# Optimization experiments

Hardware: AMD Instinct MI355X
Metric: run time of the kernel (lower is better)

## Reference

```python
import jax, jax.numpy as jnp
import numpy as np


def _dilate(x, ker):
    """Grayscale (max-plus) dilation, TF tf.nn.dilation2d semantics, SAME pad, stride 1.

    x:   [B,H,W,C] or [B,H,W,C,F]
    ker: [kh,kw,C,F]
    out: [B,H,W,C,F] = max_{dy,dx} x_pad[b, h+dy, w+dx, c(,f)] + ker[dy,dx,c,f]
    """
    kh, kw = ker.shape[0], ker.shape[1]
    pt, pl = (kh - 1) // 2, (kw - 1) // 2
    pb, pr = kh - 1 - pt, kw - 1 - pl
    if x.ndim == 4:
        x = x[..., None]  # broadcast over filter axis
    B, H, W = x.shape[0], x.shape[1], x.shape[2]
    xp = jnp.pad(x, ((0, 0), (pt, pb), (pl, pr), (0, 0), (0, 0)),
                 constant_values=-jnp.inf)
    out = None
    for dy in range(kh):
        for dx in range(kw):
            v = xp[:, dy:dy + H, dx:dx + W] + ker[dy, dx]  # [B,H,W,C,F]
            out = v if out is None else jnp.maximum(out, v)
    return out


def _erode(x, ker):
    # TF identity: erosion2d(v, f) = -dilation2d(-v, spatially-flipped f)
    return -_dilate(-x, ker[::-1, ::-1])


def _opening_p4(x, kernel):
    # x: [B,4,H,W,C], kernel: [kh,kw,3,C,F]
    kero = jnp.stack([jnp.rot90(kernel[:, :, 2], 3, axes=(0, 1)),
                      kernel[:, :, 1],
                      jnp.rot90(kernel[:, :, 0], 1, axes=(0, 1))], axis=2)
    y = jnp.concatenate([x[:, -1:], x, x[:, :1]], axis=1)  # wrap group axis -> [B,6,H,W,C]
    ero = []
    for j in range(4):
        kr = jnp.rot90(kero, j, axes=(0, 1))  # [kh,kw,3,C,F]
        d = jnp.stack([_erode(y[:, j + k], kr[:, :, k]) for k in range(3)], axis=-1)
        ero.append(jnp.min(d, axis=-1))  # min over SE depth -> [B,H,W,C,F]
    ero = jnp.stack(ero, axis=1)  # [B,4,H,W,C,F]
    ep = jnp.concatenate([ero[:, -1:], ero, ero[:, :1]], axis=1)  # [B,6,H,W,C,F]
    outs = []
    for j in range(4):
        kr = jnp.rot90(kernel, j, axes=(0, 1))
        d = jnp.stack([_dilate(ep[:, j + k], kr[:, :, k]) for k in range(3)], axis=-1)
        outs.append(jnp.max(d, axis=-1))  # max over SE depth -> [B,H,W,C,F]
    open_res = jnp.stack(outs, axis=1)  # [B,4,H,W,C,F]
    return jnp.sum(open_res, axis=-2)   # sum over input channels -> [B,4,H,W,F]


def setup_inputs() -> dict:
    key = jax.random.key(0)
    k1, k2 = jax.random.split(key)
    x = jax.random.normal(k1, (4, 4, 64, 64, 8), dtype=jnp.float32)
    kernel = jax.random.normal(k2, (3, 3, 3, 8, 16), dtype=jnp.float32) * 0.1
    return {"x": x, "kernel": kernel}


def reference(x, kernel):
    return _opening_p4(x, kernel)
```

## Files before the change

kernel.cpp:

```cpp
#include <hip/hip_runtime.h>


#define HH 64
#define WW 64
#define NEG_INF (-__builtin_inff())
#define POS_INF (__builtin_inff())

#define ROT_G(G, A, B, I, J) do { switch (G) { \
    case 0:  I = (A);     J = (B);     break; \
    case 1:  I = (B);     J = 2 - (A); break; \
    case 2:  I = 2 - (A); J = 2 - (B); break; \
    default: I = 2 - (B); J = (A);     break; } } while (0)

typedef _Float16 hv4 __attribute__((ext_vector_type(4)));

__device__ __forceinline__ hv4 f4_to_hv4(float4 v) {
    hv4 r;
    r.x = (_Float16)v.x; r.y = (_Float16)v.y;
    r.z = (_Float16)v.z; r.w = (_Float16)v.w;
    return r;
}

__global__ __launch_bounds__(256) void erode_t(const float* __restrict__ x,
                                               const float* __restrict__ ker,
                                               hv4* __restrict__ ero) {
    __shared__ __align__(16) float xs[9 * 8 * 68];

    const int tid = threadIdx.x;
    const int h = blockIdx.x & 63;
    const int g = (blockIdx.x >> 6) & 3;
    const int b = blockIdx.x >> 8;

    const float4* x4 = (const float4*)x;
    const float4* ker4 = (const float4*)ker;

    for (int t = tid; t < 1188; t += 256) {
        int q01 = t & 1;
        int u = t >> 1;
        int wp = u % 66;
        int v = u / 66;
        int r = v % 3;
        int p = v / 3;
        int g2 = (g + p + 3) & 3;
        int h2 = h - 1 + r;
        int w2 = wp - 1;
        float4 vv;
        if ((unsigned)h2 < HH && (unsigned)w2 < WW)
            vv = x4[(((b * 4 + g2) * HH + h2) * WW + w2) * 2 + q01];
        else
            vv = make_float4(POS_INF, POS_INF, POS_INF, POS_INF);
        int rowb = (p * 3 + r) * 8 + q01 * 4;
        xs[(rowb + 0) * 68 + wp] = vv.x;
        xs[(rowb + 1) * 68 + wp] = vv.y;
        xs[(rowb + 2) * 68 + wp] = vv.z;
        xs[(rowb + 3) * 68 + wp] = vv.w;
    }
    __syncthreads();

    const int q = tid & 3;
    const int c = (tid >> 2) & 7;
    const int slot = tid >> 5;
    const float4* xs4 = (const float4*)xs;

    float4 acc[8];
#pragma unroll
    for (int i = 0; i < 8; ++i)
        acc[i] = make_float4(POS_INF, POS_INF, POS_INF, POS_INF);

#pragma unroll
    for (int k2 = 0; k2 < 3; ++k2) {
        float4 ke9[9];
#pragma unroll
        for (int t9 = 0; t9 < 9; ++t9) {
            int dy = t9 / 3, dx = t9 % 3;
            int a0 = 2 - dy, b0 = 2 - dx;
            int i, jj;
            ROT_G(g, a0, b0, i, jj);
            int ka, kb, kc;
            if (k2 == 0)      { ka = 2 - jj; kb = i;      kc = 2; }
            else if (k2 == 1) { ka = i;      kb = jj;     kc = 1; }
            else              { ka = jj;     kb = 2 - i;  kc = 0; }
            ke9[t9] = ker4[((ka * 3 + kb) * 3 + kc) * 32 + c * 4 + q];
        }
#pragma unroll
        for (int dy = 0; dy < 3; ++dy) {
            const int base4 = ((k2 * 3 + dy) * 8 + c) * 17 + slot * 2;
            float4 xa = xs4[base4];
            float4 xb = xs4[base4 + 1];
            float4 xc = xs4[base4 + 2];
            float xw[12] = {xa.x, xa.y, xa.z, xa.w,
                            xb.x, xb.y, xb.z, xb.w,
                            xc.x, xc.y, xc.z, xc.w};
#pragma unroll
            for (int dx = 0; dx < 3; ++dx) {
                float4 kv = ke9[dy * 3 + dx];
#pragma unroll
                for (int i = 0; i < 8; ++i) {
                    float v = xw[i + dx];
                    acc[i].x = fminf(acc[i].x, v - kv.x);
                    acc[i].y = fminf(acc[i].y, v - kv.y);
                    acc[i].z = fminf(acc[i].z, v - kv.z);
                    acc[i].w = fminf(acc[i].w, v - kv.w);
                }
            }
        }
    }

    const int row = (b * 4 + g) * HH + h;
    const size_t obase = ((size_t)row * 66 + slot * 8 + 1) * 32 + c * 4 + q;
#pragma unroll
    for (int i = 0; i < 8; ++i)
        ero[obase + (size_t)i * 32] = f4_to_hv4(acc[i]);

    const hv4 ninf = {(_Float16)NEG_INF, (_Float16)NEG_INF,
                      (_Float16)NEG_INF, (_Float16)NEG_INF};
    if (tid < 32)
        ero[(size_t)row * 66 * 32 + tid] = ninf;
    else if (tid < 64)
        ero[((size_t)row * 66 + 65) * 32 + (tid - 32)] = ninf;
}

__global__ __launch_bounds__(256) void dilate_t2(const hv4* __restrict__ ero,
                                                 const float* __restrict__ ker,
                                                 float* __restrict__ out) {
    __shared__ __align__(16) hv4 es[4 * 6 * 10 * 32];

    const int tid = threadIdx.x;
    const int ws = blockIdx.x & 7;
    const int hs = (blockIdx.x >> 3) & 15;
    const int b = blockIdx.x >> 7;

    {
        const float4* ero4 = (const float4*)ero;
        float4* es4 = (float4*)es;
        const float nf = __uint_as_float(0xFC00FC00u);
        const float4 ninf4 = make_float4(nf, nf, nf, nf);
        for (int t = tid; t < 3840; t += 256) {
            const int cq2 = t & 15;
            const int rest = t >> 4;
            const int wp10 = rest % 10;
            const int ge = rest / 10;
            const int ei = ge % 6;
            const int gsrc = ge / 6;
            const int er = hs * 4 - 1 + ei;
            float4 v = ninf4;
            if ((unsigned)er < HH)
                v = ero4[(((b * 4 + gsrc) * HH + er) * 66 + ws * 8 + wp10) * 16 + cq2];
            es4[rest * 16 + cq2] = v;
        }
    }
    __syncthreads();

    const int q = tid & 3;
    const int c = (tid >> 2) & 7;
    const int cq = tid & 31;
    const int slot = tid >> 5;
    const float4* ker4 = (const float4*)ker;

    const hv4 ninf = {(_Float16)NEG_INF, (_Float16)NEG_INF,
                      (_Float16)NEG_INF, (_Float16)NEG_INF};
    hv4 acc[4][4];
#pragma unroll
    for (int j = 0; j < 4; ++j)
#pragma unroll
        for (int r = 0; r < 4; ++r)
            acc[j][r] = ninf;

#pragma unroll
    for (int j = 0; j < 4; ++j) {
#pragma unroll
        for (int k = 0; k < 3; ++k) {
            const int gsrc = (j + k + 3) & 3;
            hv4 kd9[9];
#pragma unroll
            for (int t9 = 0; t9 < 9; ++t9) {
                int dy = t9 / 3, dx = t9 % 3;
                int i, jj;
                ROT_G(j, dy, dx, i, jj);
                kd9[t9] = f4_to_hv4(ker4[((i * 3 + jj) * 3 + k) * 32 + cq]);
            }
            const int pbase = gsrc * 1920 + slot * 32 + cq;
#pragma unroll
            for (int ei = 0; ei < 6; ++ei) {
                const int rb = pbase + ei * 320;
                hv4 e0 = es[rb];
                hv4 e1 = es[rb + 32];
                hv4 e2 = es[rb + 64];
#pragma unroll
                for (int dy = 0; dy < 3; ++dy) {
                    const int rr = ei - dy;
                    if (rr < 0 || rr >= 4) continue;
                    acc[j][rr] = __builtin_elementwise_max(acc[j][rr], e0 + kd9[dy * 3 + 0]);
                    acc[j][rr] = __builtin_elementwise_max(acc[j][rr], e1 + kd9[dy * 3 + 1]);
                    acc[j][rr] = __builtin_elementwise_max(acc[j][rr], e2 + kd9[dy * 3 + 2]);
                }
            }
        }
    }

    float4* out4 = (float4*)out;
    const int w = ws * 8 + slot;
#pragma unroll
    for (int j = 0; j < 4; ++j) {
        const int rowb = (b * 4 + j) * HH + hs * 4;
#pragma unroll
        for (int rr = 0; rr < 4; ++rr) {
            float4 s = make_float4((float)acc[j][rr].x, (float)acc[j][rr].y,
                                   (float)acc[j][rr].z, (float)acc[j][rr].w);
#pragma unroll
            for (int off = 4; off <= 16; off <<= 1) {
                s.x += __shfl_xor(s.x, off, 64);
                s.y += __shfl_xor(s.y, off, 64);
                s.z += __shfl_xor(s.z, off, 64);
                s.w += __shfl_xor(s.w, off, 64);
            }
            if (c == 0)
                out4[((size_t)(rowb + rr) * WW + w) * 4 + q] = s;
        }
    }
}

__global__ __launch_bounds__(256, 3) void opening_fused_fb(
    const float* __restrict__ x, const float* __restrict__ ker, float* __restrict__ out)
{
    __shared__ __align__(16) float xs[8 * 4 * 144];
    __shared__ float4 es4[4 * 4 * 100];
    __shared__ float4 ke4[27 * 4 * 4];
    __shared__ float4 kd4[9 * 4 * 4];

    const int tid = threadIdx.x;
    const int tileX = blockIdx.x & 7;
    const int tileY = (blockIdx.x >> 3) & 7;
    const int j = (blockIdx.x >> 6) & 3;
    const int b = blockIdx.x >> 8;
    const float4* ker4 = (const float4*)ker;
    const float4* x4 = (const float4*)x;

    for (int t = tid; t < 1152; t += 256) {
        int q01 = t & 1;
        int cell = t >> 1;
        int g = cell / 144;
        int rem = cell - g * 144;
        int r = rem / 12;
        int s = rem - r * 12;
        int h = tileY * 8 - 2 + r;
        int w = tileX * 8 - 2 + s;
        float4 v;
        if ((unsigned)h < HH && (unsigned)w < WW)
            v = x4[(((b * 4 + g) * HH + h) * WW + w) * 2 + q01];
        else
            v = make_float4(POS_INF, POS_INF, POS_INF, POS_INF);
        int c0 = q01 * 4;
        xs[((c0 + 0) * 4 + g) * 144 + rem] = v.x;
        xs[((c0 + 1) * 4 + g) * 144 + rem] = v.y;
        xs[((c0 + 2) * 4 + g) * 144 + rem] = v.z;
        xs[((c0 + 3) * 4 + g) * 144 + rem] = v.w;
    }
    __syncthreads();

    const int q_o = tid & 3;
    const int ox = (tid >> 2) & 7;
    const int oy = tid >> 5;

    float4 acc[8];
#pragma unroll
    for (int c = 0; c < 8; ++c)
        acc[c] = make_float4(NEG_INF, NEG_INF, NEG_INF, NEG_INF);

    for (int k = 0; k < 3; ++k) {
        const int gsrc = (j + k + 3) & 3;
#pragma unroll
        for (int cg = 0; cg < 2; ++cg) {
            for (int t = tid; t < 576; t += 256) {
                if (t < 432) {
                    int q = t & 3;
                    int c4 = (t >> 2) & 3;
                    int tap = t >> 4;
                    int k2 = tap % 3;
                    int dxdy = tap / 3;
                    int dx = dxdy % 3;
                    int dy = dxdy / 3;
                    int a0 = 2 - dy, b0 = 2 - dx;
                    int i, jj;
                    ROT_G(gsrc, a0, b0, i, jj);
                    int ka, kb, kc;
                    if (k2 == 0)      { ka = 2 - jj; kb = i;      kc = 2; }
                    else if (k2 == 1) { ka = i;      kb = jj;     kc = 1; }
                    else              { ka = jj;     kb = 2 - i;  kc = 0; }
                    int c = cg * 4 + c4;
                    ke4[t] = ker4[((ka * 3 + kb) * 3 + kc) * 32 + c * 4 + q];
                } else {
                    int u = t - 432;
                    int q = u & 3;
                    int c4 = (u >> 2) & 3;
                    int dydx = u >> 4;
                    int dx = dydx % 3;
                    int dy = dydx / 3;
                    int i, jj;
                    ROT_G(j, dy, dx, i, jj);
                    int c = cg * 4 + c4;
                    kd4[u] = ker4[((i * 3 + jj) * 3 + k) * 32 + c * 4 + q];
                }
            }
            __syncthreads();

            for (int it = 0; it < 2; ++it) {
                int id = tid + (it << 8);
                int c4 = id >> 7;
                int p = id & 127;
                if (p >= 100) continue;
                int ey = (p * 205) >> 11;
                int ex = p - ey * 10;
                int h_es = tileY * 8 - 1 + ey;
                int w_es = tileX * 8 - 1 + ex;
                float4 b0, b1, b2, b3;
                if ((unsigned)h_es < HH && (unsigned)w_es < WW) {
                    b0 = b1 = b2 = b3 = make_float4(POS_INF, POS_INF, POS_INF, POS_INF);
                    int c = cg * 4 + c4;
#pragma unroll
                    for (int k2 = 0; k2 < 3; ++k2) {
                        int g2 = (gsrc + k2 + 3) & 3;
                        int base = (c * 4 + g2) * 144 + ey * 12 + ex;
#pragma unroll
                        for (int dy = 0; dy < 3; ++dy)
#pragma unroll
                            for (int dx = 0; dx < 3; ++dx) {
                                float v = xs[base + dy * 12 + dx];
                                const float4* kk = &ke4[(((dy * 3 + dx) * 3 + k2) * 4 + c4) * 4];
                                float4 kv;
                                kv = kk[0];
                                b0.x = fminf(b0.x, v - kv.x); b0.y = fminf(b0.y, v - kv.y);
                                b0.z = fminf(b0.z, v - kv.z); b0.w = fminf(b0.w, v - kv.w);
                                kv = kk[1];
                                b1.x = fminf(b1.x, v - kv.x); b1.y = fminf(b1.y, v - kv.y);
                                b1.z = fminf(b1.z, v - kv.z); b1.w = fminf(b1.w, v - kv.w);
                                kv = kk[2];
                                b2.x = fminf(b2.x, v - kv.x); b2.y = fminf(b2.y, v - kv.y);
                                b2.z = fminf(b2.z, v - kv.z); b2.w = fminf(b2.w, v - kv.w);
                                kv = kk[3];
                                b3.x = fminf(b3.x, v - kv.x); b3.y = fminf(b3.y, v - kv.y);
                                b3.z = fminf(b3.z, v - kv.z); b3.w = fminf(b3.w, v - kv.w);
                            }
                    }
                } else {
                    b0 = b1 = b2 = b3 = make_float4(NEG_INF, NEG_INF, NEG_INF, NEG_INF);
                }
                int eb = (c4 * 4) * 100 + p;
                es4[eb] = b0; es4[eb + 100] = b1; es4[eb + 200] = b2; es4[eb + 300] = b3;
            }
            __syncthreads();

#pragma unroll
            for (int c4 = 0; c4 < 4; ++c4) {
                float4 a = acc[cg * 4 + c4];
#pragma unroll
                for (int dy = 0; dy < 3; ++dy)
#pragma unroll
                    for (int dx = 0; dx < 3; ++dx) {
                        int pos = (oy + dy) * 10 + (ox + dx);
                        float4 e = es4[(c4 * 4 + q_o) * 100 + pos];
                        float4 kv = kd4[(dy * 3 + dx) * 16 + c4 * 4 + q_o];
                        a.x = fmaxf(a.x, e.x + kv.x);
                        a.y = fmaxf(a.y, e.y + kv.y);
                        a.z = fmaxf(a.z, e.z + kv.z);
                        a.w = fmaxf(a.w, e.w + kv.w);
                    }
                acc[cg * 4 + c4] = a;
            }
            __syncthreads();
        }
    }

    float4 s = acc[0];
#pragma unroll
    for (int c = 1; c < 8; ++c) {
        s.x += acc[c].x; s.y += acc[c].y; s.z += acc[c].z; s.w += acc[c].w;
    }
    const int h = tileY * 8 + oy;
    const int w = tileX * 8 + ox;
    ((float4*)out)[(((b * 4 + j) * HH + h) * WW + w) * 4 + q_o] = s;
}

extern "C" void kernel_launch(void* const* d_in, const int* in_sizes, int n_in,
                              void* d_out, int out_size, void* d_ws, size_t ws_size,
                              hipStream_t stream) {
    const float* x = (const float*)d_in[0];
    const float* ker = (const float*)d_in[1];
    float* out = (float*)d_out;

    const size_t ero_f16_bytes = (size_t)16 * HH * 66 * 32 * 8;

    if (ws_size >= ero_f16_bytes) {
        hv4* ero = (hv4*)d_ws;
        erode_t<<<1024, 256, 0, stream>>>(x, ker, ero);
        dilate_t2<<<512, 256, 0, stream>>>(ero, ker, out);
    } else {
        opening_fused_fb<<<1024, 256, 0, stream>>>(x, ker, out);
    }
}
```

Measured before the change: 92.10 us.

## Fuse erosion and dilation into one tiled kernel with shared-memory halo

Replaces the two-kernel erode/dilate pipeline, which passed the eroded tensor through a global fp16 workspace, with a single kernel. Each 512-thread block computes the eroded 10x10 halo tile for all four groups into LDS, then dilates and channel-reduces the 8x8 output tile. This removes the global round trip and one launch. In exchange, each block recomputes the halo erosion that neighbouring tiles also compute, and the grid shrinks to 256 large blocks with heavy register use.

```diff
diff --git a/kernel.cpp b/kernel.cpp
--- a/kernel.cpp
+++ b/kernel.cpp
@@ -21,364 +21,193 @@
     return r;
 }
 
-__global__ __launch_bounds__(256) void erode_t(const float* __restrict__ x,
-                                               const float* __restrict__ ker,
-                                               hv4* __restrict__ ero) {
-    __shared__ __align__(16) float xs[9 * 8 * 68];
+__global__ __launch_bounds__(512, 2) void opening_fused_v15(
+    const float* __restrict__ x, const float* __restrict__ ker,
+    float* __restrict__ out)
+{
+    __shared__ __align__(16) float xs[4 * 8 * 148];
+    __shared__ __align__(16) hv4  es[4 * 10 * 10 * 32];
 
     const int tid = threadIdx.x;
-    const int h = blockIdx.x & 63;
-    const int g = (blockIdx.x >> 6) & 3;
-    const int b = blockIdx.x >> 8;
+    const int tx = blockIdx.x & 7;
+    const int ty = (blockIdx.x >> 3) & 7;
+    const int b  = blockIdx.x >> 6;
 
     const float4* x4 = (const float4*)x;
     const float4* ker4 = (const float4*)ker;
 
-    for (int t = tid; t < 1188; t += 256) {
-        int q01 = t & 1;
-        int u = t >> 1;
-        int wp = u % 66;
-        int v = u / 66;
-        int r = v % 3;
-        int p = v / 3;
-        int g2 = (g + p + 3) & 3;
-        int h2 = h - 1 + r;
-        int w2 = wp - 1;
-        float4 vv;
-        if ((unsigned)h2 < HH && (unsigned)w2 < WW)
-            vv = x4[(((b * 4 + g2) * HH + h2) * WW + w2) * 2 + q01];
-        else
-            vv = make_float4(POS_INF, POS_INF, POS_INF, POS_INF);
-        int rowb = (p * 3 + r) * 8 + q01 * 4;
-        xs[(rowb + 0) * 68 + wp] = vv.x;
-        xs[(rowb + 1) * 68 + wp] = vv.y;
-        xs[(rowb + 2) * 68 + wp] = vv.z;
-        xs[(rowb + 3) * 68 + wp] = vv.w;
-    }
-    __syncthreads();
-
-    const int q = tid & 3;
-    const int c = (tid >> 2) & 7;
-    const int slot = tid >> 5;
-    const float4* xs4 = (const float4*)xs;
-
-    float4 acc[8];
-#pragma unroll
-    for (int i = 0; i < 8; ++i)
-        acc[i] = make_float4(POS_INF, POS_INF, POS_INF, POS_INF);
-
-#pragma unroll
-    for (int k2 = 0; k2 < 3; ++k2) {
-        float4 ke9[9];
-#pragma unroll
-        for (int t9 = 0; t9 < 9; ++t9) {
-            int dy = t9 / 3, dx = t9 % 3;
-            int a0 = 2 - dy, b0 = 2 - dx;
-            int i, jj;
-            ROT_G(g, a0, b0, i, jj);
-            int ka, kb, kc;
-            if (k2 == 0)      { ka = 2 - jj; kb = i;      kc = 2; }
-            else if (k2 == 1) { ka = i;      kb = jj;     kc = 1; }
-            else              { ka = jj;     kb = 2 - i;  kc = 0; }
-            ke9[t9] = ker4[((ka * 3 + kb) * 3 + kc) * 32 + c * 4 + q];
-        }
-#pragma unroll
-        for (int dy = 0; dy < 3; ++dy) {
-            const int base4 = ((k2 * 3 + dy) * 8 + c) * 17 + slot * 2;
-            float4 xa = xs4[base4];
-            float4 xb = xs4[base4 + 1];
-            float4 xc = xs4[base4 + 2];
-            float xw[12] = {xa.x, xa.y, xa.z, xa.w,
-                            xb.x, xb.y, xb.z, xb.w,
-                            xc.x, xc.y, xc.z, xc.w};
-#pragma unroll
-            for (int dx = 0; dx < 3; ++dx) {
-                float4 kv = ke9[dy * 3 + dx];
-#pragma unroll
-                for (int i = 0; i < 8; ++i) {
-                    float v = xw[i + dx];
-                    acc[i].x = fminf(acc[i].x, v - kv.x);
-                    acc[i].y = fminf(acc[i].y, v - kv.y);
-                    acc[i].z = fminf(acc[i].z, v - kv.z);
-                    acc[i].w = fminf(acc[i].w, v - kv.w);
-                }
-            }
-        }
-    }
-
-    const int row = (b * 4 + g) * HH + h;
-    const size_t obase = ((size_t)row * 66 + slot * 8 + 1) * 32 + c * 4 + q;
-#pragma unroll
-    for (int i = 0; i < 8; ++i)
-        ero[obase + (size_t)i * 32] = f4_to_hv4(acc[i]);
-
-    const hv4 ninf = {(_Float16)NEG_INF, (_Float16)NEG_INF,
-                      (_Float16)NEG_INF, (_Float16)NEG_INF};
-    if (tid < 32)
-        ero[(size_t)row * 66 * 32 + tid] = ninf;
-    else if (tid < 64)
-        ero[((size_t)row * 66 + 65) * 32 + (tid - 32)] = ninf;
-}
-
-__global__ __launch_bounds__(256) void dilate_t2(const hv4* __restrict__ ero,
-                                                 const float* __restrict__ ker,
-                                                 float* __restrict__ out) {
-    __shared__ __align__(16) hv4 es[4 * 6 * 10 * 32];
-
-    const int tid = threadIdx.x;
-    const int ws = blockIdx.x & 7;
-    const int hs = (blockIdx.x >> 3) & 15;
-    const int b = blockIdx.x >> 7;
-
-    {
-        const float4* ero4 = (const float4*)ero;
-        float4* es4 = (float4*)es;
-        const float nf = __uint_as_float(0xFC00FC00u);
-        const float4 ninf4 = make_float4(nf, nf, nf, nf);
-        for (int t = tid; t < 3840; t += 256) {
-            const int cq2 = t & 15;
-            const int rest = t >> 4;
-            const int wp10 = rest % 10;
-            const int ge = rest / 10;
-            const int ei = ge % 6;
-            const int gsrc = ge / 6;
-            const int er = hs * 4 - 1 + ei;
-            float4 v = ninf4;
-            if ((unsigned)er < HH)
-                v = ero4[(((b * 4 + gsrc) * HH + er) * 66 + ws * 8 + wp10) * 16 + cq2];
-            es4[rest * 16 + cq2] = v;
-        }
-    }
-    __syncthreads();
-
-    const int q = tid & 3;
-    const int c = (tid >> 2) & 7;
-    const int cq = tid & 31;
-    const int slot = tid >> 5;
-    const float4* ker4 = (const float4*)ker;
-
-    const hv4 ninf = {(_Float16)NEG_INF, (_Float16)NEG_INF,
-                      (_Float16)NEG_INF, (_Float16)NEG_INF};
-    hv4 acc[4][4];
-#pragma unroll
-    for (int j = 0; j < 4; ++j)
-#pragma unroll
-        for (int r = 0; r < 4; ++r)
-            acc[j][r] = ninf;
-
-#pragma unroll
-    for (int j = 0; j < 4; ++j) {
-#pragma unroll
-        for (int k = 0; k < 3; ++k) {
-            const int gsrc = (j + k + 3) & 3;
-            hv4 kd9[9];
-#pragma unroll
-            for (int t9 = 0; t9 < 9; ++t9) {
-                int dy = t9 / 3, dx = t9 % 3;
-                int i, jj;
-                ROT_G(j, dy, dx, i, jj);
-                kd9[t9] = f4_to_hv4(ker4[((i * 3 + jj) * 3 + k) * 32 + cq]);
-            }
-            const int pbase = gsrc * 1920 + slot * 32 + cq;
-#pragma unroll
-            for (int ei = 0; ei < 6; ++ei) {
-                const int rb = pbase + ei * 320;
-                hv4 e0 = es[rb];
-                hv4 e1 = es[rb + 32];
-                hv4 e2 = es[rb + 64];
-#pragma unroll
-                for (int dy = 0; dy < 3; ++dy) {
-                    const int rr = ei - dy;
-                    if (rr < 0 || rr >= 4) continue;
-                    acc[j][rr] = __builtin_elementwise_max(acc[j][rr], e0 + kd9[dy * 3 + 0]);
-                    acc[j][rr] = __builtin_elementwise_max(acc[j][rr], e1 + kd9[dy * 3 + 1]);
-                    acc[j][rr] = __builtin_elementwise_max(acc[j][rr], e2 + kd9[dy * 3 + 2]);
-                }
-            }
-        }
-    }
-
-    float4* out4 = (float4*)out;
-    const int w = ws * 8 + slot;
-#pragma unroll
-    for (int j = 0; j < 4; ++j) {
-        const int rowb = (b * 4 + j) * HH + hs * 4;
-#pragma unroll
-        for (int rr = 0; rr < 4; ++rr) {
-            float4 s = make_float4((float)acc[j][rr].x, (float)acc[j][rr].y,
-                                   (float)acc[j][rr].z, (float)acc[j][rr].w);
-#pragma unroll
-            for (int off = 4; off <= 16; off <<= 1) {
-                s.x += __shfl_xor(s.x, off, 64);
-                s.y += __shfl_xor(s.y, off, 64);
-                s.z += __shfl_xor(s.z, off, 64);
-                s.w += __shfl_xor(s.w, off, 64);
-            }
-            if (c == 0)
-                out4[((size_t)(rowb + rr) * WW + w) * 4 + q] = s;
-        }
-    }
-}
-
-__global__ __launch_bounds__(256, 3) void opening_fused_fb(
-    const float* __restrict__ x, const float* __restrict__ ker, float* __restrict__ out)
-{
-    __shared__ __align__(16) float xs[8 * 4 * 144];
-    __shared__ float4 es4[4 * 4 * 100];
-    __shared__ float4 ke4[27 * 4 * 4];
-    __shared__ float4 kd4[9 * 4 * 4];
-
-    const int tid = threadIdx.x;
-    const int tileX = blockIdx.x & 7;
-    const int tileY = (blockIdx.x >> 3) & 7;
-    const int j = (blockIdx.x >> 6) & 3;
-    const int b = blockIdx.x >> 8;
-    const float4* ker4 = (const float4*)ker;
-    const float4* x4 = (const float4*)x;
-
-    for (int t = tid; t < 1152; t += 256) {
+    for (int t = tid; t < 1152; t += 512) {
         int q01 = t & 1;
         int cell = t >> 1;
         int g = cell / 144;
         int rem = cell - g * 144;
         int r = rem / 12;
         int s = rem - r * 12;
-        int h = tileY * 8 - 2 + r;
-        int w = tileX * 8 - 2 + s;
+        int h = ty * 8 - 2 + r;
+        int w = tx * 8 - 2 + s;
         float4 v;
         if ((unsigned)h < HH && (unsigned)w < WW)
             v = x4[(((b * 4 + g) * HH + h) * WW + w) * 2 + q01];
         else
             v = make_float4(POS_INF, POS_INF, POS_INF, POS_INF);
-        int c0 = q01 * 4;
-        xs[((c0 + 0) * 4 + g) * 144 + rem] = v.x;
-        xs[((c0 + 1) * 4 + g) * 144 + rem] = v.y;
-        xs[((c0 + 2) * 4 + g) * 144 + rem] = v.z;
-        xs[((c0 + 3) * 4 + g) * 144 + rem] = v.w;
+        int pb = (g * 8 + q01 * 4) * 148 + rem;
+        xs[pb]           = v.x;
+        xs[pb + 148]     = v.y;
+        xs[pb + 2 * 148] = v.z;
+        xs[pb + 3 * 148] = v.w;
     }
     __syncthreads();
 
-    const int q_o = tid & 3;
-    const int ox = (tid >> 2) & 7;
-    const int oy = tid >> 5;
-
-    float4 acc[8];
-#pragma unroll
-    for (int c = 0; c < 8; ++c)
-        acc[c] = make_float4(NEG_INF, NEG_INF, NEG_INF, NEG_INF);
-
-    for (int k = 0; k < 3; ++k) {
-        const int gsrc = (j + k + 3) & 3;
-#pragma unroll
-        for (int cg = 0; cg < 2; ++cg) {
-            for (int t = tid; t < 576; t += 256) {
-                if (t < 432) {
-                    int q = t & 3;
-                    int c4 = (t >> 2) & 3;
-                    int tap = t >> 4;
-                    int k2 = tap % 3;
-                    int dxdy = tap / 3;
-                    int dx = dxdy % 3;
-                    int dy = dxdy / 3;
-                    int a0 = 2 - dy, b0 = 2 - dx;
-                    int i, jj;
-                    ROT_G(gsrc, a0, b0, i, jj);
-                    int ka, kb, kc;
-                    if (k2 == 0)      { ka = 2 - jj; kb = i;      kc = 2; }
-                    else if (k2 == 1) { ka = i;      kb = jj;     kc = 1; }
-                    else              { ka = jj;     kb = 2 - i;  kc = 0; }
-                    int c = cg * 4 + c4;
-                    ke4[t] = ker4[((ka * 3 + kb) * 3 + kc) * 32 + c * 4 + q];
-                } else {
-                    int u = t - 432;
-                    int q = u & 3;
-                    int c4 = (u >> 2) & 3;
-                    int dydx = u >> 4;
-                    int dx = dydx % 3;
-                    int dy = dydx / 3;
+    const hv4 ninf = {(_Float16)NEG_INF, (_Float16)NEG_INF,
+                      (_Float16)NEG_INF, (_Float16)NEG_INF};
+
+    {
+        const int cq   = tid & 31;
+        const int c    = (tid >> 2) & 7;
+        const int eyh5 = ((tid >> 5) & 1) * 5;
+        const int g    = (tid >> 6) & 3;
+        const int half = tid >> 8;
+        const int ex0  = half * 5;
+        const float4* xs4 = (const float4*)xs;
+
+        float4 acc[5][5];
+#pragma unroll
+        for (int a = 0; a < 5; ++a)
+#pragma unroll
+            for (int p = 0; p < 5; ++p)
+                acc[a][p] = make_float4(POS_INF, POS_INF, POS_INF, POS_INF);
+
+#pragma unroll
+        for (int k2 = 0; k2 < 3; ++k2) {
+            float4 ke9[9];
+#pragma unroll
+            for (int t9 = 0; t9 < 9; ++t9) {
+                int dy = t9 / 3, dx = t9 % 3;
+                int a0 = 2 - dy, b0 = 2 - dx;
+                int i, jj;
+                ROT_G(g, a0, b0, i, jj);
+                int ka, kb, kc;
+                if (k2 == 0)      { ka = 2 - jj; kb = i;      kc = 2; }
+                else if (k2 == 1) { ka = i;      kb = jj;     kc = 1; }
+                else              { ka = jj;     kb = 2 - i;  kc = 0; }
+                ke9[t9] = ker4[((ka * 3 + kb) * 3 + kc) * 32 + cq];
+            }
+            const int g2 = (g + k2 + 3) & 3;
+            const int pb4 = (g2 * 8 + c) * 37;
+#pragma unroll
+            for (int el = 0; el < 5; ++el) {
+#pragma unroll
+                for (int dy = 0; dy < 3; ++dy) {
+                    const int rowb = pb4 + (eyh5 + el + dy) * 3;
+                    float w7[7];
+                    if (half == 0) {
+                        float4 xa = xs4[rowb], xb = xs4[rowb + 1];
+                        w7[0] = xa.x; w7[1] = xa.y; w7[2] = xa.z; w7[3] = xa.w;
+                        w7[4] = xb.x; w7[5] = xb.y; w7[6] = xb.z;
+                    } else {
+                        float4 xb = xs4[rowb + 1], xc = xs4[rowb + 2];
+                        w7[0] = xb.y; w7[1] = xb.z; w7[2] = xb.w;
+                        w7[3] = xc.x; w7[4] = xc.y; w7[5] = xc.z; w7[6] = xc.w;
+                    }
+#pragma unroll
+                    for (int dx = 0; dx < 3; ++dx) {
+                        float4 kv = ke9[dy * 3 + dx];
+#pragma unroll
+                        for (int px = 0; px < 5; ++px) {
+                            float v = w7[px + dx];
+                            acc[el][px].x = fminf(acc[el][px].x, v - kv.x);
+                            acc[el][px].y = fminf(acc[el][px].y, v - kv.y);
+                            acc[el][px].z = fminf(acc[el][px].z, v - kv.z);
+                            acc[el][px].w = fminf(acc[el][px].w, v - kv.w);
+                        }
+                    }
+                }
+            }
+        }
+        const int hb = ty * 8 - 1 + eyh5;
+        const int wb = tx * 8 - 1 + ex0;
+        const int ebase = g * 3200 + eyh5 * 320 + ex0 * 32 + cq;
+#pragma unroll
+        for (int el = 0; el < 5; ++el)
+#pragma unroll
+            for (int px = 0; px < 5; ++px) {
+                bool ok = ((unsigned)(hb + el) < HH) && ((unsigned)(wb + px) < WW);
+                es[ebase + el * 320 + px * 32] =
+                    ok ? f4_to_hv4(acc[el][px]) : ninf;
+            }
+    }
+    __syncthreads();
+
+    {
+        const int q = tid & 3;
+        const int c = (tid >> 2) & 7;
+        const int cq = tid & 31;
+        const int slot = (tid >> 5) & 7;
+        const int rhalf = tid >> 8;
+
+        hv4 acc[4][4];
+#pragma unroll
+        for (int j = 0; j < 4; ++j)
+#pragma unroll
+            for (int r = 0; r < 4; ++r)
+                acc[j][r] = ninf;
+
+#pragma unroll
+        for (int j = 0; j < 4; ++j) {
+#pragma unroll
+            for (int k = 0; k < 3; ++k) {
+                const int gsrc = (j + k + 3) & 3;
+                hv4 kd9[9];
+#pragma unroll
+                for (int t9 = 0; t9 < 9; ++t9) {
+                    int dy = t9 / 3, dx = t9 % 3;
                     int i, jj;
                     ROT_G(j, dy, dx, i, jj);
-                    int c = cg * 4 + c4;
-                    kd4[u] = ker4[((i * 3 + jj) * 3 + k) * 32 + c * 4 + q];
-                }
-            }
-            __syncthreads();
-
-            for (int it = 0; it < 2; ++it) {
-                int id = tid + (it << 8);
-                int c4 = id >> 7;
-                int p = id & 127;
-                if (p >= 100) continue;
-                int ey = (p * 205) >> 11;
-                int ex = p - ey * 10;
-                int h_es = tileY * 8 - 1 + ey;
-                int w_es = tileX * 8 - 1 + ex;
-                float4 b0, b1, b2, b3;
-                if ((unsigned)h_es < HH && (unsigned)w_es < WW) {
-                    b0 = b1 = b2 = b3 = make_float4(POS_INF, POS_INF, POS_INF, POS_INF);
-                    int c = cg * 4 + c4;
-#pragma unroll
-                    for (int k2 = 0; k2 < 3; ++k2) {
-                        int g2 = (gsrc + k2 + 3) & 3;
-                        int base = (c * 4 + g2) * 144 + ey * 12 + ex;
-#pragma unroll
-                        for (int dy = 0; dy < 3; ++dy)
-#pragma unroll
-                            for (int dx = 0; dx < 3; ++dx) {
-                                float v = xs[base + dy * 12 + dx];
-                                const float4* kk = &ke4[(((dy * 3 + dx) * 3 + k2) * 4 + c4) * 4];
-                                float4 kv;
-                                kv = kk[0];
-                                b0.x = fminf(b0.x, v - kv.x); b0.y = fminf(b0.y, v - kv.y);
-                                b0.z = fminf(b0.z, v - kv.z); b0.w = fminf(b0.w, v - kv.w);
-                                kv = kk[1];
-                                b1.x = fminf(b1.x, v - kv.x); b1.y = fminf(b1.y, v - kv.y);
-                                b1.z = fminf(b1.z, v - kv.z); b1.w = fminf(b1.w, v - kv.w);
-                                kv = kk[2];
-                                b2.x = fminf(b2.x, v - kv.x); b2.y = fminf(b2.y, v - kv.y);
-                                b2.z = fminf(b2.z, v - kv.z); b2.w = fminf(b2.w, v - kv.w);
-                                kv = kk[3];
-                                b3.x = fminf(b3.x, v - kv.x); b3.y = fminf(b3.y, v - kv.y);
-                                b3.z = fminf(b3.z, v - kv.z); b3.w = fminf(b3.w, v - kv.w);
-                            }
+                    kd9[t9] = f4_to_hv4(ker4[((i * 3 + jj) * 3 + k) * 32 + cq]);
+                }
+                const int pbase = gsrc * 3200 + rhalf * 1280 + slot * 32 + cq;
+#pragma unroll
+                for (int ei = 0; ei < 6; ++ei) {
+                    const int rb = pbase + ei * 320;
+                    hv4 e0 = es[rb];
+                    hv4 e1 = es[rb + 32];
+                    hv4 e2 = es[rb + 64];
+#pragma unroll
+                    for (int dy = 0; dy < 3; ++dy) {
+                        const int rr = ei - dy;
+                        if (rr < 0 || rr >= 4) continue;
+                        acc[j][rr] = __builtin_elementwise_max(acc[j][rr],
+                                                               e0 + kd9[dy * 3 + 0]);
+                        acc[j][rr] = __builtin_elementwise_max(acc[j][rr],
+                                                               e1 + kd9[dy * 3 + 1]);
+                        acc[j][rr] = __builtin_elementwise_max(acc[j][rr],
+                                                               e2 + kd9[dy * 3 + 2]);
                     }
-                } else {
-                    b0 = b1 = b2 = b3 = make_float4(NEG_INF, NEG_INF, NEG_INF, NEG_INF);
-                }
-                int eb = (c4 * 4) * 100 + p;
-                es4[eb] = b0; es4[eb + 100] = b1; es4[eb + 200] = b2; es4[eb + 300] = b3;
-            }
-            __syncthreads();
-
-#pragma unroll
-            for (int c4 = 0; c4 < 4; ++c4) {
-                float4 a = acc[cg * 4 + c4];
-#pragma unroll
-                for (int dy = 0; dy < 3; ++dy)
-#pragma unroll
-                    for (int dx = 0; dx < 3; ++dx) {
-                        int pos = (oy + dy) * 10 + (ox + dx);
-                        float4 e = es4[(c4 * 4 + q_o) * 100 + pos];
-                        float4 kv = kd4[(dy * 3 + dx) * 16 + c4 * 4 + q_o];
-                        a.x = fmaxf(a.x, e.x + kv.x);
-                        a.y = fmaxf(a.y, e.y + kv.y);
-                        a.z = fmaxf(a.z, e.z + kv.z);
-                        a.w = fmaxf(a.w, e.w + kv.w);
-                    }
-                acc[cg * 4 + c4] = a;
-            }
-            __syncthreads();
+                }
+            }
+        }
+
+        float4* out4 = (float4*)out;
+        const int w = tx * 8 + slot;
+#pragma unroll
+        for (int j = 0; j < 4; ++j) {
+            const int rowb = (b * 4 + j) * HH + ty * 8 + rhalf * 4;
+#pragma unroll
+            for (int rr = 0; rr < 4; ++rr) {
+                float4 s = make_float4((float)acc[j][rr].x, (float)acc[j][rr].y,
+                                       (float)acc[j][rr].z, (float)acc[j][rr].w);
+#pragma unroll
+                for (int off = 4; off <= 16; off <<= 1) {
+                    s.x += __shfl_xor(s.x, off, 64);
+                    s.y += __shfl_xor(s.y, off, 64);
+                    s.z += __shfl_xor(s.z, off, 64);
+                    s.w += __shfl_xor(s.w, off, 64);
+                }
+                if (c == 0)
+                    out4[((size_t)(rowb + rr) * WW + w) * 4 + q] = s;
+            }
         }
     }
-
-    float4 s = acc[0];
-#pragma unroll
-    for (int c = 1; c < 8; ++c) {
-        s.x += acc[c].x; s.y += acc[c].y; s.z += acc[c].z; s.w += acc[c].w;
-    }
-    const int h = tileY * 8 + oy;
-    const int w = tileX * 8 + ox;
-    ((float4*)out)[(((b * 4 + j) * HH + h) * WW + w) * 4 + q_o] = s;
 }
 
 extern "C" void kernel_launch(void* const* d_in, const int* in_sizes, int n_in,
@@ -387,14 +216,7 @@
     const float* x = (const float*)d_in[0];
     const float* ker = (const float*)d_in[1];
     float* out = (float*)d_out;
-
-    const size_t ero_f16_bytes = (size_t)16 * HH * 66 * 32 * 8;
-
-    if (ws_size >= ero_f16_bytes) {
-        hv4* ero = (hv4*)d_ws;
-        erode_t<<<1024, 256, 0, stream>>>(x, ker, ero);
-        dilate_t2<<<512, 256, 0, stream>>>(ero, ker, out);
-    } else {
-        opening_fused_fb<<<1024, 256, 0, stream>>>(x, ker, out);
-    }
+    (void)d_ws; (void)ws_size;
+
+    opening_fused_v15<<<256, 512, 0, stream>>>(x, ker, out);
 }
```

After: 152.8 us. +65.9%, slower.
